# Optimization experiments

Measured on AMD Instinct MI355X. Metric: run time of the kernel, lower is better.

## Reference

```python
import jax, jax.numpy as jnp
import numpy as np

MAXDISP = 48  # init kwarg
KS = list(range(3, 12))  # window sizes 3..11 -> channel prefixes k*k (9..121)


def setup_inputs() -> dict:
    key = jax.random.key(0)
    k1, k2 = jax.random.split(key)
    B, C, H, W = 2, 121, 128, 256
    x = jax.random.normal(k1, (B, C, H, W), dtype=jnp.float32)
    y = jax.random.normal(k2, (B, C, H, W), dtype=jnp.float32)
    return {"x": x, "y": y}


def reference(x, y):
    # GetCostVolume forward (attack=True branch: mean |x - shifted y| over
    # nested channel prefixes idx=k*k, k=3..11, for each disparity shift).
    # Note: the attack=False branch replaces |x-y| with (x!=y).float(); for
    # continuous random inputs that is identically 1, so we implement the
    # differentiable abs-diff branch, which has identical loop/memory structure.
    B, C, H, W = x.shape
    ksq = jnp.array([k * k for k in KS], dtype=x.dtype)          # (9,) divisors
    prefix_idx = jnp.array([k * k - 1 for k in KS])              # cumsum gather idx
    wpos = jnp.arange(W)

    def body(carry, d):
        # shift y right by d along width; region w<d is masked to zero below,
        # matching cost[..., :d] = 0 from the torch zeros-init.
        y_sh = jnp.roll(y, d, axis=-1)                           # (B,C,H,W)
        diff = jnp.abs(x - y_sh)                                 # (B,C,H,W)
        csum = jnp.cumsum(diff, axis=1)                          # prefix sums over channels
        means = csum[:, prefix_idx] / ksq[:, None, None]         # (B,9,H,W)
        means = jnp.where(wpos >= d, means, jnp.zeros((), x.dtype))
        return carry, means

    _, cost = jax.lax.scan(body, None, jnp.arange(MAXDISP))      # (D,B,9,H,W)
    return jnp.transpose(cost, (1, 2, 0, 3, 4))                  # (B,9,D,H,W)
```

## Files before the change

kernel.cpp:

```cpp
#include <hip/hip_runtime.h>

#define B_ 2
#define C_ 121
#define H_ 128
#define W_ 256
#define D_ 48
#define CT 11
#define NCHUNK 11
#define NT 256
#define NDY 4
#define YROW 312
#define ZS 3

typedef float f32x4 __attribute__((ext_vector_type(4)));
typedef const void __attribute__((address_space(1)))* gas1_t;
typedef void __attribute__((address_space(3)))* las3_t;

__launch_bounds__(NT)
__global__ void cost_volume_kernel(const float* __restrict__ xg,
                                   const float* __restrict__ yg,
                                   float* __restrict__ out)
{
    __shared__ __align__(16) float YLS[2][CT][YROW];

    const int t  = threadIdx.x;
    const int h  = blockIdx.x;
    const int b  = blockIdx.y;
    const int z  = blockIdx.z;
    const int wq = t & 63;
    const int wv = t >> 6;
    const int d0 = z * 16 + wv * NDY;
    const int w0 = wq * 4;

    for (int i = t; i < 2 * CT * 48; i += NT) {
        int nb = i / (CT * 48);
        int r  = i % (CT * 48);
        YLS[nb][r / 48][r % 48] = 0.0f;
    }

    constexpr int HW = H_ * W_;
    const size_t row0 = (((size_t)b * C_) * H_ + h) * (size_t)W_;
    const float* xp = xg + row0 + w0;

    auto stage = [&](int chunk, int nb) {
        for (int i = wv; i < CT; i += 4) {
            const int c = chunk * CT + i;
            __builtin_amdgcn_global_load_lds(
                (gas1_t)(yg + row0 + (size_t)c * HW + (size_t)wq * 4),
                (las3_t)&YLS[nb][i][48], 16, 0, 0);
        }
    };

    float acc[NDY][4];
    #pragma unroll
    for (int jd = 0; jd < NDY; ++jd)
        #pragma unroll
        for (int jw = 0; jw < 4; ++jw) acc[jd][jw] = 0.0f;

    stage(0, 0);
    __syncthreads();

    const int bp = w0 - d0 + 44;

    for (int k = 0; k < NCHUNK; ++k) {
        const int cur = k & 1;

        f32x4 xq[CT];
        #pragma unroll
        for (int cc = 0; cc < CT; ++cc)
            xq[cc] = *(const f32x4*)(xp + (size_t)(k * CT + cc) * HW);

        if (k + 1 < NCHUNK) stage(k + 1, cur ^ 1);

        #pragma unroll
        for (int cc = 0; cc < CT; ++cc) {
            float yw[8];
            *(f32x4*)&yw[0] = *(const f32x4*)&YLS[cur][cc][bp];
            *(f32x4*)&yw[4] = *(const f32x4*)&YLS[cur][cc][bp + 4];

            const float xvv[4] = {xq[cc].x, xq[cc].y, xq[cc].z, xq[cc].w};
            #pragma unroll
            for (int jd = 0; jd < NDY; ++jd)
                #pragma unroll
                for (int jw = 0; jw < 4; ++jw)
                    acc[jd][jw] += __builtin_fabsf(xvv[jw] - yw[4 + jw - jd]);

            #pragma unroll
            for (int bi = 0; bi < 9; ++bi) {
                constexpr int KB[9] = {8, 15, 24, 35, 48, 63, 80, 99, 120};
                const int bc = KB[bi];
                if (k * CT + cc == bc) {
                    const float inv = 1.0f / (float)(bc + 1);
                    const size_t obase = (((size_t)b * 9 + bi) * D_) * (size_t)HW
                                       + (size_t)h * W_ + (size_t)w0;
                    #pragma unroll
                    for (int jd = 0; jd < NDY; ++jd) {
                        const int d = d0 + jd;
                        f32x4 v;
                        v.x = (w0 + 0 >= d) ? acc[jd][0] * inv : 0.0f;
                        v.y = (w0 + 1 >= d) ? acc[jd][1] * inv : 0.0f;
                        v.z = (w0 + 2 >= d) ? acc[jd][2] * inv : 0.0f;
                        v.w = (w0 + 3 >= d) ? acc[jd][3] * inv : 0.0f;
                        __builtin_nontemporal_store(v,
                            (f32x4*)&out[obase + (size_t)d * HW]);
                    }
                }
            }
        }
        __syncthreads();
    }
}

extern "C" void kernel_launch(void* const* d_in, const int* in_sizes, int n_in,
                              void* d_out, int out_size, void* d_ws, size_t ws_size,
                              hipStream_t stream)
{
    const float* x = (const float*)d_in[0];
    const float* y = (const float*)d_in[1];
    float* o = (float*)d_out;
    dim3 grid(H_, B_, ZS);
    dim3 block(NT, 1, 1);
    hipLaunchKernelGGL(cost_volume_kernel, grid, block, 0, stream, x, y, o);
}
```

Before: 55.89 us.

## Stage x into LDS alongside y with two-deep async prefetch pipeline

Both the x and y channel rows are now loaded into double-buffered LDS with global_load_lds, replacing the direct register loads of x. Two chunks are issued before the loop, and each step waits with explicit vmcnt counts and raw barriers, so the next-but-one chunk streams in while the current one is computed. The change also sets an occupancy hint in launch bounds and switches the output stores from nontemporal to normal. This costs extra LDS per block and relies on hand-counted vmcnt values that must match how many loads each wave issues.

Result: faster. 52.80 us (-5.5%).

```diff
diff --git a/kernel.cpp b/kernel.cpp
--- a/kernel.cpp
+++ b/kernel.cpp
@@ -9,18 +9,25 @@
 #define NCHUNK 11
 #define NT 256
 #define NDY 4
+#define ZS 3
+#define XROW 264
 #define YROW 312
-#define ZS 3
+
+constexpr int HW = H_ * W_;
 
 typedef float f32x4 __attribute__((ext_vector_type(4)));
 typedef const void __attribute__((address_space(1)))* gas1_t;
 typedef void __attribute__((address_space(3)))* las3_t;
 
-__launch_bounds__(NT)
+#define VMWAIT(NSTR) asm volatile("s_waitcnt vmcnt(" NSTR ")" ::: "memory")
+#define CFENCE()     asm volatile("" ::: "memory")
+
+__launch_bounds__(NT, 3)
 __global__ void cost_volume_kernel(const float* __restrict__ xg,
                                    const float* __restrict__ yg,
                                    float* __restrict__ out)
 {
+    __shared__ __align__(16) float XLS[2][CT][XROW];
     __shared__ __align__(16) float YLS[2][CT][YROW];
 
     const int t  = threadIdx.x;
@@ -31,6 +38,7 @@
     const int wv = t >> 6;
     const int d0 = z * 16 + wv * NDY;
     const int w0 = wq * 4;
+    const int bp = w0 - d0 + 44;
 
     for (int i = t; i < 2 * CT * 48; i += NT) {
         int nb = i / (CT * 48);
@@ -38,47 +46,47 @@
         YLS[nb][r / 48][r % 48] = 0.0f;
     }
 
-    constexpr int HW = H_ * W_;
     const size_t row0 = (((size_t)b * C_) * H_ + h) * (size_t)W_;
-    const float* xp = xg + row0 + w0;
+    const float* xrow = xg + row0 + (size_t)wq * 4;
+    const float* yrow = yg + row0 + (size_t)wq * 4;
 
     auto stage = [&](int chunk, int nb) {
-        for (int i = wv; i < CT; i += 4) {
-            const int c = chunk * CT + i;
-            __builtin_amdgcn_global_load_lds(
-                (gas1_t)(yg + row0 + (size_t)c * HW + (size_t)wq * 4),
-                (las3_t)&YLS[nb][i][48], 16, 0, 0);
+        for (int i = wv; i < 2 * CT; i += 4) {
+            const int cc = i >> 1;
+            const size_t off = (size_t)(chunk * CT + cc) * HW;
+            if (i & 1)
+                __builtin_amdgcn_global_load_lds((gas1_t)(yrow + off),
+                                                 (las3_t)&YLS[nb][cc][48], 16, 0, 0);
+            else
+                __builtin_amdgcn_global_load_lds((gas1_t)(xrow + off),
+                                                 (las3_t)&XLS[nb][cc][0], 16, 0, 0);
         }
     };
 
-    float acc[NDY][4];
-    #pragma unroll
-    for (int jd = 0; jd < NDY; ++jd)
-        #pragma unroll
-        for (int jw = 0; jw < 4; ++jw) acc[jd][jw] = 0.0f;
+    stage(0, 0);
+    stage(1, 1);
 
-    stage(0, 0);
-    __syncthreads();
-
-    const int bp = w0 - d0 + 44;
+    float acc[NDY][4] = {};
 
     for (int k = 0; k < NCHUNK; ++k) {
         const int cur = k & 1;
 
-        f32x4 xq[CT];
-        #pragma unroll
-        for (int cc = 0; cc < CT; ++cc)
-            xq[cc] = *(const f32x4*)(xp + (size_t)(k * CT + cc) * HW);
-
-        if (k + 1 < NCHUNK) stage(k + 1, cur ^ 1);
+        if (k < NCHUNK - 1) {
+            if (wv < 2) VMWAIT("6"); else VMWAIT("5");
+        } else {
+            VMWAIT("0");
+        }
+        __builtin_amdgcn_s_barrier();
+        CFENCE();
 
         #pragma unroll
         for (int cc = 0; cc < CT; ++cc) {
+            const f32x4 xv = *(const f32x4*)&XLS[cur][cc][w0];
             float yw[8];
             *(f32x4*)&yw[0] = *(const f32x4*)&YLS[cur][cc][bp];
             *(f32x4*)&yw[4] = *(const f32x4*)&YLS[cur][cc][bp + 4];
 
-            const float xvv[4] = {xq[cc].x, xq[cc].y, xq[cc].z, xq[cc].w};
+            const float xvv[4] = {xv.x, xv.y, xv.z, xv.w};
             #pragma unroll
             for (int jd = 0; jd < NDY; ++jd)
                 #pragma unroll
@@ -88,9 +96,8 @@
             #pragma unroll
             for (int bi = 0; bi < 9; ++bi) {
                 constexpr int KB[9] = {8, 15, 24, 35, 48, 63, 80, 99, 120};
-                const int bc = KB[bi];
-                if (k * CT + cc == bc) {
-                    const float inv = 1.0f / (float)(bc + 1);
+                if (k * CT + cc == KB[bi]) {
+                    const float inv = 1.0f / (float)(KB[bi] + 1);
                     const size_t obase = (((size_t)b * 9 + bi) * D_) * (size_t)HW
                                        + (size_t)h * W_ + (size_t)w0;
                     #pragma unroll
@@ -101,13 +108,17 @@
                         v.y = (w0 + 1 >= d) ? acc[jd][1] * inv : 0.0f;
                         v.z = (w0 + 2 >= d) ? acc[jd][2] * inv : 0.0f;
                         v.w = (w0 + 3 >= d) ? acc[jd][3] * inv : 0.0f;
-                        __builtin_nontemporal_store(v,
-                            (f32x4*)&out[obase + (size_t)d * HW]);
+                        *(f32x4*)&out[obase + (size_t)d * HW] = v;
                     }
                 }
             }
         }
-        __syncthreads();
+
+        if (k + 2 < NCHUNK) {
+            CFENCE();
+            __builtin_amdgcn_s_barrier();
+            stage(k + 2, cur);
+        }
     }
 }
 
```
